# Optimization experiments

Hardware: AMD Instinct MI355X
Metric: run time of the kernel (lower is better)

Reference implementation:

```python
import jax, jax.numpy as jnp
import numpy as np

DIM = 2048
NUM_HEADS = 16
HEAD_DIM = DIM // NUM_HEADS
ROPE_BASE = 10000.0


def _rope_cache(seq_len):
    inv_freq = 1.0 / (ROPE_BASE ** (jnp.arange(0, HEAD_DIM, 2, dtype=jnp.float32) / HEAD_DIM))
    t = jnp.arange(seq_len, dtype=jnp.float32)
    freqs = jnp.einsum('i,j->ij', t, inv_freq)          # [S, HEAD_DIM//2]
    emb = jnp.concatenate([freqs, freqs], axis=-1)       # [S, HEAD_DIM]
    return jnp.cos(emb), jnp.sin(emb)


def _rotate_half(x):
    x1, x2 = jnp.split(x, 2, axis=-1)
    return jnp.concatenate([-x2, x1], axis=-1)


def setup_inputs() -> dict:
    key = jax.random.key(0)
    kx, kq, ko = jax.random.split(key, 3)
    B, S = 2, 2048
    x = jax.random.normal(kx, (B, S, DIM), dtype=jnp.float32)
    # torch nn.Linear(dim, 3*dim) weight has shape [3*dim, dim]; y = x @ W.T
    w_qkv = jax.random.normal(kq, (3 * DIM, DIM), dtype=jnp.float32) * (DIM ** -0.5)
    w_out = jax.random.normal(ko, (DIM, DIM), dtype=jnp.float32) * (DIM ** -0.5)
    return {"x": x, "w_qkv": w_qkv, "w_out": w_out}


def reference(x, w_qkv, w_out):
    B, S, _ = x.shape
    qkv = x @ w_qkv.T                                   # [B, S, 3*DIM]
    q, k, v = jnp.split(qkv, 3, axis=-1)
    def to_heads(t):
        return t.reshape(B, S, NUM_HEADS, HEAD_DIM).transpose(0, 2, 1, 3)  # [B, H, S, d]
    q, k, v = to_heads(q), to_heads(k), to_heads(v)

    cos, sin = _rope_cache(S)                           # [S, d]
    cos = cos[None, None, :, :]
    sin = sin[None, None, :, :]
    q = q * cos + _rotate_half(q) * sin
    k = k * cos + _rotate_half(k) * sin

    scale = HEAD_DIM ** -0.5
    scores = jnp.einsum('bhqd,bhkd->bhqk', q, k) * scale  # [B, H, S, S]
    causal = jnp.tril(jnp.ones((S, S), dtype=bool))
    scores = jnp.where(causal[None, None], scores, -jnp.inf)
    attn = jax.nn.softmax(scores, axis=-1)
    out = jnp.einsum('bhqk,bhkd->bhqd', attn, v)          # [B, H, S, d]
    out = out.transpose(0, 2, 1, 3).reshape(B, S, DIM)
    return out @ w_out.T
```

## Files before the change

### kernel.cpp

```cpp
#include <hip/hip_runtime.h>
#include <cstdint>
#include <cstddef>

#define NHEADS 16
#define HDIM   128
#define BATCH  2
#define SEQ    2048
#define DMODEL 2048
#define MTOT   (BATCH*SEQ)
#define NQKV   (3*DMODEL)

typedef __attribute__((ext_vector_type(8))) __bf16 bf16x8;
typedef __attribute__((ext_vector_type(4))) float f32x4;
typedef __attribute__((ext_vector_type(8))) unsigned short ushort8v;

__device__ __forceinline__ unsigned short f2bf(float f){
  __bf16 h = (__bf16)f;
  return __builtin_bit_cast(unsigned short, h);
}
__device__ __forceinline__ float bf2f(unsigned short s){
  return __uint_as_float(((uint32_t)s) << 16);
}
__device__ __forceinline__ void gload_lds16(const void* src, void* lds_base){
  __builtin_amdgcn_global_load_lds((const __attribute__((address_space(1))) unsigned int*)src,
                                   (__attribute__((address_space(3))) unsigned int*)lds_base,
                                   16, 0, 0);
}

template<int CTRL>
__device__ __forceinline__ float dppmv(float x){
  return __uint_as_float((unsigned)__builtin_amdgcn_update_dpp(
      0, (int)__float_as_uint(x), CTRL, 0xF, 0xF, true));
}
__device__ __forceinline__ float rmax16(float x){
  x = fmaxf(x, dppmv<0x128>(x));
  x = fmaxf(x, dppmv<0x124>(x));
  x = fmaxf(x, dppmv<0x122>(x));
  x = fmaxf(x, dppmv<0x121>(x));
  return x;
}
__device__ __forceinline__ float rsum16(float x){
  x += dppmv<0x128>(x);
  x += dppmv<0x124>(x);
  x += dppmv<0x122>(x);
  x += dppmv<0x121>(x);
  return x;
}

__global__ void cast3_kernel(const float* __restrict__ s0, unsigned short* __restrict__ d0, int n0,
                             const float* __restrict__ s1, unsigned short* __restrict__ d1, int n1,
                             const float* __restrict__ s2, unsigned short* __restrict__ d2, int n2){
  const int stride = gridDim.x*blockDim.x*8;
  const int base = (blockIdx.x*blockDim.x + threadIdx.x)*8;
  #pragma unroll 1
  for (int a = 0; a < 3; ++a){
    const float* s = a==0 ? s0 : (a==1 ? s1 : s2);
    unsigned short* d = a==0 ? d0 : (a==1 ? d1 : d2);
    const int n = a==0 ? n0 : (a==1 ? n1 : n2);
    for (int i = base; i < n; i += stride){
      float4 x = *reinterpret_cast<const float4*>(s + i);
      float4 y = *reinterpret_cast<const float4*>(s + i + 4);
      ushort8v o;
      o[0]=f2bf(x.x); o[1]=f2bf(x.y); o[2]=f2bf(x.z); o[3]=f2bf(x.w);
      o[4]=f2bf(y.x); o[5]=f2bf(y.y); o[6]=f2bf(y.z); o[7]=f2bf(y.w);
      *reinterpret_cast<ushort8v*>(d + i) = o;
    }
  }
}

template<int MODE>
__global__ __launch_bounds__(512, 2) void gemm2(
    const unsigned short* __restrict__ A,
    const unsigned short* __restrict__ Bw,
    float* __restrict__ Cf,
    unsigned short* __restrict__ qo,
    unsigned short* __restrict__ ko,
    unsigned short* __restrict__ vo,
    int M, int N, int K)
{
  __shared__ __align__(16) unsigned short smem[49152];
  auto lds = reinterpret_cast<unsigned short (*)[3][128*64]>(smem);

  const int lane = threadIdx.x & 63;
  const int wid  = threadIdx.x >> 6;
  const int wm = wid >> 2, wn = wid & 3;
  const int hi = lane >> 4;
  const int l15 = lane & 15;

  const int nwg = gridDim.x * gridDim.y;
  const int bid = blockIdx.y * gridDim.x + blockIdx.x;
  const int swz = (bid & 7) * (nwg >> 3) + (bid >> 3);
  const int by = swz & 31;
  const int bx = swz >> 5;
  const int m0 = by * 128;
  const int n0 = bx * 256;

  const int NT = K >> 6;

  auto stage = [&](const unsigned short* base, int row0, int k0, int buf, int slot){
    const int rlo = wid << 4;
    #pragma unroll
    for (int i=0;i<2;++i){
      const int r = rlo + i*8 + (lane>>3);
      const int csrc = ((lane&7) ^ (lane>>3)) << 3;
      gload_lds16(base + (size_t)(row0 + r)*K + k0 + csrc,
                  &lds[buf][slot][(rlo + i*8)*64]);
    }
  };
  auto frag = [&](const unsigned short* h, int r, int s){
    return *reinterpret_cast<const bf16x8*>(h + r*64 + ((s ^ (r&7)) << 3));
  };

  f32x4 acc[4][4];
  #pragma unroll
  for (int i=0;i<4;++i)
    #pragma unroll
    for (int j=0;j<4;++j) acc[i][j] = (f32x4){0.f,0.f,0.f,0.f};

  stage(A,  m0,      0, 0, 0);
  stage(Bw, n0,      0, 0, 1);
  stage(Bw, n0+128,  0, 0, 2);
  if (NT > 1){
    stage(A, m0, 64, 1, 0);
    asm volatile("s_waitcnt vmcnt(2)" ::: "memory");
  } else {
    asm volatile("s_waitcnt vmcnt(0)" ::: "memory");
  }
  __builtin_amdgcn_sched_barrier(0);
  __builtin_amdgcn_s_barrier();

  bf16x8 Ar[4][2];
  bf16x8 Br[2][2];

  auto tile_body = [&](int kt, int cur){
    const int nxt = cur ^ 1;
    const unsigned short* Ah = &lds[cur][0][0];
    const unsigned short* Bh = &lds[cur][1 + (wn>>1)][0];
    const int rbase = (wn & 1) * 64;

    #pragma unroll
    for (int fm=0;fm<4;++fm)
      #pragma unroll
      for (int kk=0;kk<2;++kk)
        Ar[fm][kk] = frag(Ah, wm*64 + fm*16 + l15, kk*4 + hi);
    #pragma unroll
    for (int nf=0;nf<2;++nf)
      #pragma unroll
      for (int kk=0;kk<2;++kk)
        Br[nf][kk] = frag(Bh, rbase + nf*16 + l15, kk*4 + hi);
    if (kt+1 < NT){
      stage(Bw, n0,     (kt+1)*64, nxt, 1);
      stage(Bw, n0+128, (kt+1)*64, nxt, 2);
    }
    asm volatile("s_waitcnt lgkmcnt(8)" ::: "memory");
    __builtin_amdgcn_sched_barrier(0);
    __builtin_amdgcn_s_barrier();
    asm volatile("s_waitcnt lgkmcnt(0)" ::: "memory");
    __builtin_amdgcn_sched_barrier(0);
    __builtin_amdgcn_s_setprio(1);
    #pragma unroll
    for (int fm=0;fm<4;++fm){
      acc[fm][0] = __builtin_amdgcn_mfma_f32_16x16x32_bf16(Ar[fm][0], Br[0][0], acc[fm][0], 0,0,0);
      acc[fm][0] = __builtin_amdgcn_mfma_f32_16x16x32_bf16(Ar[fm][1], Br[0][1], acc[fm][0], 0,0,0);
      acc[fm][1] = __builtin_amdgcn_mfma_f32_16x16x32_bf16(Ar[fm][0], Br[1][0], acc[fm][1], 0,0,0);
      acc[fm][1] = __builtin_amdgcn_mfma_f32_16x16x32_bf16(Ar[fm][1], Br[1][1], acc[fm][1], 0,0,0);
    }
    __builtin_amdgcn_s_setprio(0);
    __builtin_amdgcn_sched_barrier(0);
    __builtin_amdgcn_s_barrier();

    #pragma unroll
    for (int nf=0;nf<2;++nf)
      #pragma unroll
      for (int kk=0;kk<2;++kk)
        Br[nf][kk] = frag(Bh, rbase + 32 + nf*16 + l15, kk*4 + hi);
    if (kt+2 < NT) stage(A, m0, (kt+2)*64, cur, 0);
    __builtin_amdgcn_sched_barrier(0);
    __builtin_amdgcn_s_barrier();
    asm volatile("s_waitcnt lgkmcnt(0)" ::: "memory");
    __builtin_amdgcn_sched_barrier(0);
    __builtin_amdgcn_s_setprio(1);
    #pragma unroll
    for (int fm=0;fm<4;++fm){
      acc[fm][2] = __builtin_amdgcn_mfma_f32_16x16x32_bf16(Ar[fm][0], Br[0][0], acc[fm][2], 0,0,0);
      acc[fm][2] = __builtin_amdgcn_mfma_f32_16x16x32_bf16(Ar[fm][1], Br[0][1], acc[fm][2], 0,0,0);
      acc[fm][3] = __builtin_amdgcn_mfma_f32_16x16x32_bf16(Ar[fm][0], Br[1][0], acc[fm][3], 0,0,0);
      acc[fm][3] = __builtin_amdgcn_mfma_f32_16x16x32_bf16(Ar[fm][1], Br[1][1], acc[fm][3], 0,0,0);
    }
    __builtin_amdgcn_s_setprio(0);
    if (kt+2 < NT)      asm volatile("s_waitcnt vmcnt(2)" ::: "memory");
    else if (kt+1 < NT) asm volatile("s_waitcnt vmcnt(0)" ::: "memory");
    __builtin_amdgcn_sched_barrier(0);
    __builtin_amdgcn_s_barrier();
  };

  for (int kt2 = 0; kt2 < NT; kt2 += 2){
    tile_body(kt2,     0);
    tile_body(kt2 + 1, 1);
  }

  if (MODE == 0 && (n0 >> 11) == 2){
    __builtin_amdgcn_s_barrier();
    unsigned short* trsp = smem;
    #pragma unroll
    for (int fm=0;fm<4;++fm){
      const int srow = wm*64 + fm*16 + hi*4;
      #pragma unroll
      for (int p=0;p<4;++p){
        const int dcol = wn*64 + p*16 + l15;
        f32x4 v = acc[fm][p];
        ushort4 pk;
        pk.x=f2bf(v[0]); pk.y=f2bf(v[1]); pk.z=f2bf(v[2]); pk.w=f2bf(v[3]);
        *reinterpret_cast<ushort4*>(trsp + dcol*136 + srow) = pk;
      }
    }
    __syncthreads();
    const int bb  = m0 >> 11;
    const int ss0 = m0 & 2047;
    const size_t vrow = (size_t)(bb*2048 + (n0 - 4096));
    const int t = threadIdx.x;
    #pragma unroll
    for (int it=0; it<8; ++it){
      const int dl = it*32 + (t>>4);
      const int ch = t & 15;
      ushort8v val = *reinterpret_cast<const ushort8v*>(trsp + dl*136 + ch*8);
      *reinterpret_cast<ushort8v*>(vo + (vrow + dl)*SEQ + ss0 + ch*8) = val;
    }
  } else {
    #pragma unroll
    for (int fm=0;fm<4;++fm){
      const int row0 = m0 + wm*64 + fm*16 + (hi<<2);
      #pragma unroll
      for (int p=0;p<4;++p){
        const int col = n0 + wn*64 + p*16 + l15;
        f32x4 v = acc[fm][p];
        if (MODE == 1){
          #pragma unroll
          for (int r=0;r<4;++r) Cf[(size_t)(row0+r)*N + col] = v[r];
        } else {
          const int part = col >> 11;
          const int hh = (col >> 7) & 15;
          const int d  = col & 127;
          const int bb = row0 >> 11;
          const int ss = row0 & 2047;
          unsigned short* base = (part == 0 ? qo : ko)
                               + ((size_t)(bb*NHEADS+hh)*SEQ + ss)*HDIM + d;
          #pragma unroll
          for (int r=0;r<4;++r) base[r*HDIM] = f2bf(v[r]);
        }
      }
    }
  }
}

__global__ void rope_kernel(unsigned short* __restrict__ qh, unsigned short* __restrict__ kh){
  const int idx = blockIdx.x * blockDim.x + threadIdx.x;
  const int j  = idx & 63;
  const int s  = (idx >> 6) & 2047;
  const int bh = (idx >> 17) & 31;
  const int t  = idx >> 22;
  unsigned short* base = (t ? kh : qh) + ((size_t)bh*SEQ + s)*HDIM;
  const float x1 = bf2f(base[j]);
  const float x2 = bf2f(base[j+64]);
  const float inv = exp2f(-(float)j * (13.287712379549449f/64.f));
  const float ang = (float)s * inv;
  float sn, cs;
  sincosf(ang, &sn, &cs);
  float o1 = x1*cs - x2*sn;
  float o2 = x2*cs + x1*sn;
  const float QSCALE = 0.08838834764831845f * 1.4426950408889634f;
  if (t == 0){ o1 *= QSCALE; o2 *= QSCALE; }
  base[j]    = f2bf(o1);
  base[j+64] = f2bf(o2);
}

__global__ __launch_bounds__(256, 2) void attn_kernel(
    const unsigned short* __restrict__ qh,
    const unsigned short* __restrict__ kh,
    const unsigned short* __restrict__ vT,
    unsigned short* __restrict__ ao)
{
  __shared__ __align__(16) unsigned short Ks[2][64*128];
  __shared__ __align__(16) unsigned short Vs[2][128*64];
  __shared__ __align__(16) unsigned short Ps[4][16*64];

  const int lane = threadIdx.x & 63;
  const int wid  = threadIdx.x >> 6;
  const int hi   = lane >> 4;
  const int l15  = lane & 15;
  const int pr = blockIdx.x;
  const int bh = blockIdx.y;
  const int b_ = bh >> 4, h_ = bh & 15;

  const unsigned short* Qb = qh + (size_t)bh * SEQ * HDIM;
  const unsigned short* Kb = kh + (size_t)bh * SEQ * HDIM;
  const unsigned short* Vb = vT + (size_t)bh * HDIM * SEQ;

  const int qrowf[2] = { pr*64 + wid*16, (31-pr)*64 + wid*16 };

  auto stageKV = [&](int kg, int buf){
    #pragma unroll
    for (int i=0;i<4;++i){
      const int r  = (wid*4+i)*4 + (lane>>4);
      const int cb = ((lane&15)<<4) ^ ((r&7)<<4);
      gload_lds16(Kb + (size_t)(kg*64 + r)*HDIM + (cb>>1), &Ks[buf][0] + (wid*4+i)*512);
    }
    #pragma unroll
    for (int i=0;i<4;++i){
      const int d  = (wid*4+i)*8 + (lane>>3);
      const int cb = ((lane&7)<<4) ^ ((d&7)<<4);
      gload_lds16(Vb + (size_t)d*SEQ + kg*64 + (cb>>1), &Vs[buf][0] + (wid*4+i)*512);
    }
  };

  bf16x8 qf[2][4];
  #pragma unroll
  for (int fi=0; fi<2; ++fi){
    const int qr = qrowf[fi] + l15;
    #pragma unroll
    for (int ks = 0; ks < 4; ++ks)
      qf[fi][ks] = *reinterpret_cast<const bf16x8*>(Qb + (size_t)qr*HDIM + ks*32 + hi*8);
  }

  f32x4 oacc[2][8];
  #pragma unroll
  for (int fi=0;fi<2;++fi)
    #pragma unroll
    for (int t=0;t<8;++t) oacc[fi][t] = (f32x4){0.f,0.f,0.f,0.f};
  float mrun[2][4], lrun[2][4];
  #pragma unroll
  for (int fi=0;fi<2;++fi)
    #pragma unroll
    for (int r=0;r<4;++r){ mrun[fi][r] = -3.0e38f; lrun[fi][r] = 0.f; }

  const int nkt = 32 - pr;

  stageKV(0, 0);
  __syncthreads();

  for (int kt = 0; kt < nkt; ++kt){
    const int cur = kt & 1;
    if (kt + 1 < nkt) stageKV(kt + 1, cur ^ 1);

    const bool lo_act = (kt <= pr);

    f32x4 sacc[2][4];
    #pragma unroll
    for (int fi=0;fi<2;++fi)
      #pragma unroll
      for (int nt=0;nt<4;++nt) sacc[fi][nt] = (f32x4){0.f,0.f,0.f,0.f};
    __builtin_amdgcn_s_setprio(1);
    #pragma unroll
    for (int nt=0;nt<4;++nt){
      const int krow = nt*16 + l15;
      bf16x8 kf[4];
      #pragma unroll
      for (int ks=0;ks<4;++ks){
        const int cb = (ks*64 + (hi<<4)) ^ ((krow&7)<<4);
        kf[ks] = *reinterpret_cast<const bf16x8*>(&Ks[cur][0] + krow*128 + (cb>>1));
      }
      #pragma unroll
      for (int ks=0;ks<4;++ks)
        sacc[1][nt] = __builtin_amdgcn_mfma_f32_16x16x32_bf16(qf[1][ks], kf[ks], sacc[1][nt], 0,0,0);
      if (lo_act){
        #pragma unroll
        for (int ks=0;ks<4;++ks)
          sacc[0][nt] = __builtin_amdgcn_mfma_f32_16x16x32_bf16(qf[0][ks], kf[ks], sacc[0][nt], 0,0,0);
      }
    }
    __builtin_amdgcn_s_setprio(0);

    char* pb = (char*)&Ps[wid][0];
    #pragma unroll
    for (int fi=0; fi<2; ++fi){
      if (fi == 0 && !lo_act) continue;

      if (kt*64 + 63 > qrowf[fi]){
        #pragma unroll
        for (int nt=0;nt<4;++nt){
          const int key = kt*64 + nt*16 + l15;
          #pragma unroll
          for (int r=0;r<4;++r){
            const int qr = qrowf[fi] + hi*4 + r;
            if (key > qr) sacc[fi][nt][r] = -1.0e30f;
          }
        }
      }

      float fac[4];
      #pragma unroll
      for (int r=0;r<4;++r){
        float mx = fmaxf(fmaxf(sacc[fi][0][r], sacc[fi][1][r]),
                         fmaxf(sacc[fi][2][r], sacc[fi][3][r]));
        mx = rmax16(mx);
        const float mnew = fmaxf(mrun[fi][r], mx);
        fac[r] = exp2f(mrun[fi][r] - mnew);
        mrun[fi][r] = mnew;
        float ps = 0.f;
        #pragma unroll
        for (int nt=0;nt<4;++nt){
          const float p = exp2f(sacc[fi][nt][r] - mnew);
          sacc[fi][nt][r] = p;
          ps += p;
        }
        ps = rsum16(ps);
        lrun[fi][r] = lrun[fi][r]*fac[r] + ps;
      }
      #pragma unroll
      for (int t=0;t<8;++t)
        #pragma unroll
        for (int r=0;r<4;++r) oacc[fi][t][r] *= fac[r];

      #pragma unroll
      for (int nt=0;nt<4;++nt){
        const int keyb = (nt*16 + l15) << 1;
        #pragma unroll
        for (int r=0;r<4;++r){
          const int prow = hi*4 + r;
          *(unsigned short*)(pb + prow*128 + (keyb ^ ((prow&7)<<4))) = f2bf(sacc[fi][nt][r]);
        }
      }
      asm volatile("s_waitcnt lgkmcnt(0)" ::: "memory");
      __builtin_amdgcn_sched_barrier(0);

      bf16x8 pa[2];
      {
        const int prow = l15;
        #pragma unroll
        for (int ks=0;ks<2;++ks){
          const int pcb = (ks*64 + (hi<<4)) ^ ((prow&7)<<4);
          pa[ks] = *reinterpret_cast<const bf16x8*>(pb + prow*128 + pcb);
        }
      }
      __builtin_amdgcn_s_setprio(1);
      #pragma unroll
      for (int ks=0;ks<2;++ks){
        #pragma unroll
        for (int t=0;t<8;++t){
          const int drow = t*16 + l15;
          const int vcb = (ks*64 + (hi<<4)) ^ ((drow&7)<<4);
          bf16x8 vb = *reinterpret_cast<const bf16x8*>(&Vs[cur][0] + drow*64 + (vcb>>1));
          oacc[fi][t] = __builtin_amdgcn_mfma_f32_16x16x32_bf16(pa[ks], vb, oacc[fi][t], 0,0,0);
        }
      }
      __builtin_amdgcn_s_setprio(0);
    }

    __syncthreads();
  }

  #pragma unroll
  for (int fi=0;fi<2;++fi){
    float linv[4];
    #pragma unroll
    for (int r=0;r<4;++r) linv[r] = 1.0f / lrun[fi][r];
    #pragma unroll
    for (int t=0;t<8;++t){
      const int col = h_*HDIM + t*16 + l15;
      #pragma unroll
      for (int r=0;r<4;++r){
        const int s_ = qrowf[fi] + hi*4 + r;
        ao[(size_t)(b_*SEQ + s_)*DMODEL + col] = f2bf(oacc[fi][t][r] * linv[r]);
      }
    }
  }
}

extern "C" void kernel_launch(void* const* d_in, const int* in_sizes, int n_in,
                              void* d_out, int out_size, void* d_ws, size_t ws_size,
                              hipStream_t stream)
{
  const float* x     = (const float*)d_in[0];
  const float* w_qkv = (const float*)d_in[1];
  const float* w_out = (const float*)d_in[2];
  float* out = (float*)d_out;

  unsigned short* xb    = (unsigned short*)d_ws;
  unsigned short* wqkvb = xb    + (size_t)MTOT*DMODEL;
  unsigned short* woutb = wqkvb + (size_t)NQKV*DMODEL;
  unsigned short* qhb   = woutb + (size_t)DMODEL*DMODEL;
  unsigned short* khb   = qhb   + (size_t)MTOT*DMODEL;
  unsigned short* vtb   = khb   + (size_t)MTOT*DMODEL;
  unsigned short* aob   = vtb   + (size_t)MTOT*DMODEL;

  hipLaunchKernelGGL(cast3_kernel, dim3(1024), dim3(256), 0, stream,
                     x, xb, MTOT*DMODEL, w_qkv, wqkvb, NQKV*DMODEL, w_out, woutb, DMODEL*DMODEL);
  hipLaunchKernelGGL((gemm2<0>), dim3(NQKV/256, MTOT/128), dim3(512), 0, stream,
                     xb, wqkvb, (float*)nullptr, qhb, khb, vtb, MTOT, NQKV, DMODEL);
  hipLaunchKernelGGL(rope_kernel, dim3((2*BATCH*NHEADS*SEQ*64)/256), dim3(256), 0, stream, qhb, khb);
  hipLaunchKernelGGL(attn_kernel, dim3(16, BATCH*NHEADS), dim3(256), 0, stream, qhb, khb, vtb, aob);
  hipLaunchKernelGGL((gemm2<1>), dim3(DMODEL/256, MTOT/128), dim3(512), 0, stream,
                     aob, woutb, out, (unsigned short*)nullptr, (unsigned short*)nullptr,
                     (unsigned short*)nullptr, MTOT, DMODEL, DMODEL);
}
```

Measured before the change: 262.6 us.

## Add pipelined 128x128 output-projection GEMM and lazy softmax rescaling

Adds a dedicated output-projection GEMM kernel with 128x128 tiles, 256 threads, double-buffered LDS staging via direct global-to-LDS loads, split MFMA phases with priority hints and an XCD-aware block swizzle. It replaces the previous 256-wide gemm2<1> launch so the 4096x2048 output GEMM uses more workgroups. Separately, the attention softmax now skips the running-max rescale of the O accumulator and row sum unless some row's max grows by more than 8 (log2 units), which removes per-tile multiplies at the cost of letting unnormalized exponentials grow up to 2^8. The swizzle hardcodes 32 row-blocks, so the new GEMM assumes M=4096.

```diff
diff --git a/kernel.cpp b/kernel.cpp
--- a/kernel.cpp
+++ b/kernel.cpp
@@ -249,6 +249,140 @@
           for (int r=0;r<4;++r) base[r*HDIM] = f2bf(v[r]);
         }
       }
+    }
+  }
+}
+
+__global__ __launch_bounds__(256, 2) void gemm_op(
+    const unsigned short* __restrict__ A,
+    const unsigned short* __restrict__ Bw,
+    float* __restrict__ Cf,
+    int M, int N, int K)
+{
+  __shared__ __align__(16) unsigned short smem[2][2][128*64];
+  const int lane = threadIdx.x & 63;
+  const int wid  = threadIdx.x >> 6;
+  const int wm = wid >> 1, wn = wid & 1;
+  const int hi = lane >> 4;
+  const int l15 = lane & 15;
+
+  const int nwg = gridDim.x * gridDim.y;
+  const int bid = blockIdx.y * gridDim.x + blockIdx.x;
+  const int swz = (bid & 7) * (nwg >> 3) + (bid >> 3);
+  const int by = swz & 31;
+  const int bx = swz >> 5;
+  const int m0 = by * 128;
+  const int n0 = bx * 128;
+
+  const int NT = K >> 6;
+
+  auto stage = [&](const unsigned short* base, int row0, int k0, int buf, int slot){
+    const int rlo = wid << 5;
+    #pragma unroll
+    for (int i=0;i<4;++i){
+      const int r = rlo + i*8 + (lane>>3);
+      const int csrc = ((lane&7) ^ (lane>>3)) << 3;
+      gload_lds16(base + (size_t)(row0 + r)*K + k0 + csrc,
+                  &smem[buf][slot][(rlo + i*8)*64]);
+    }
+  };
+  auto frag = [&](const unsigned short* h, int r, int s){
+    return *reinterpret_cast<const bf16x8*>(h + r*64 + ((s ^ (r&7)) << 3));
+  };
+
+  f32x4 acc[4][4];
+  #pragma unroll
+  for (int i=0;i<4;++i)
+    #pragma unroll
+    for (int j=0;j<4;++j) acc[i][j] = (f32x4){0.f,0.f,0.f,0.f};
+
+  stage(A,  m0, 0, 0, 0);
+  stage(Bw, n0, 0, 0, 1);
+  if (NT > 1){
+    stage(A, m0, 64, 1, 0);
+    asm volatile("s_waitcnt vmcnt(4)" ::: "memory");
+  } else {
+    asm volatile("s_waitcnt vmcnt(0)" ::: "memory");
+  }
+  __builtin_amdgcn_sched_barrier(0);
+  __builtin_amdgcn_s_barrier();
+
+  bf16x8 Ar[4][2];
+  bf16x8 Br[2][2];
+
+  auto tile_body = [&](int kt, int cur){
+    const int nxt = cur ^ 1;
+    const unsigned short* Ah = &smem[cur][0][0];
+    const unsigned short* Bh = &smem[cur][1][0];
+    const int rbase = wn * 64;
+
+    #pragma unroll
+    for (int fm=0;fm<4;++fm)
+      #pragma unroll
+      for (int kk=0;kk<2;++kk)
+        Ar[fm][kk] = frag(Ah, wm*64 + fm*16 + l15, kk*4 + hi);
+    #pragma unroll
+    for (int nf=0;nf<2;++nf)
+      #pragma unroll
+      for (int kk=0;kk<2;++kk)
+        Br[nf][kk] = frag(Bh, rbase + nf*16 + l15, kk*4 + hi);
+    if (kt+1 < NT) stage(Bw, n0, (kt+1)*64, nxt, 1);
+    asm volatile("s_waitcnt lgkmcnt(8)" ::: "memory");
+    __builtin_amdgcn_sched_barrier(0);
+    __builtin_amdgcn_s_barrier();
+    asm volatile("s_waitcnt lgkmcnt(0)" ::: "memory");
+    __builtin_amdgcn_sched_barrier(0);
+    __builtin_amdgcn_s_setprio(1);
+    #pragma unroll
+    for (int fm=0;fm<4;++fm){
+      acc[fm][0] = __builtin_amdgcn_mfma_f32_16x16x32_bf16(Ar[fm][0], Br[0][0], acc[fm][0], 0,0,0);
+      acc[fm][0] = __builtin_amdgcn_mfma_f32_16x16x32_bf16(Ar[fm][1], Br[0][1], acc[fm][0], 0,0,0);
+      acc[fm][1] = __builtin_amdgcn_mfma_f32_16x16x32_bf16(Ar[fm][0], Br[1][0], acc[fm][1], 0,0,0);
+      acc[fm][1] = __builtin_amdgcn_mfma_f32_16x16x32_bf16(Ar[fm][1], Br[1][1], acc[fm][1], 0,0,0);
+    }
+    __builtin_amdgcn_s_setprio(0);
+    __builtin_amdgcn_sched_barrier(0);
+    __builtin_amdgcn_s_barrier();
+
+    #pragma unroll
+    for (int nf=0;nf<2;++nf)
+      #pragma unroll
+      for (int kk=0;kk<2;++kk)
+        Br[nf][kk] = frag(Bh, rbase + 32 + nf*16 + l15, kk*4 + hi);
+    if (kt+2 < NT) stage(A, m0, (kt+2)*64, cur, 0);
+    __builtin_amdgcn_sched_barrier(0);
+    __builtin_amdgcn_s_barrier();
+    asm volatile("s_waitcnt lgkmcnt(0)" ::: "memory");
+    __builtin_amdgcn_sched_barrier(0);
+    __builtin_amdgcn_s_setprio(1);
+    #pragma unroll
+    for (int fm=0;fm<4;++fm){
+      acc[fm][2] = __builtin_amdgcn_mfma_f32_16x16x32_bf16(Ar[fm][0], Br[0][0], acc[fm][2], 0,0,0);
+      acc[fm][2] = __builtin_amdgcn_mfma_f32_16x16x32_bf16(Ar[fm][1], Br[0][1], acc[fm][2], 0,0,0);
+      acc[fm][3] = __builtin_amdgcn_mfma_f32_16x16x32_bf16(Ar[fm][0], Br[1][0], acc[fm][3], 0,0,0);
+      acc[fm][3] = __builtin_amdgcn_mfma_f32_16x16x32_bf16(Ar[fm][1], Br[1][1], acc[fm][3], 0,0,0);
+    }
+    __builtin_amdgcn_s_setprio(0);
+    if (kt+2 < NT)      asm volatile("s_waitcnt vmcnt(4)" ::: "memory");
+    else if (kt+1 < NT) asm volatile("s_waitcnt vmcnt(0)" ::: "memory");
+    __builtin_amdgcn_sched_barrier(0);
+    __builtin_amdgcn_s_barrier();
+  };
+
+  for (int kt2 = 0; kt2 < NT; kt2 += 2){
+    tile_body(kt2,     0);
+    tile_body(kt2 + 1, 1);
+  }
+
+  #pragma unroll
+  for (int fm=0;fm<4;++fm){
+    const int row0 = m0 + wm*64 + fm*16 + (hi<<2);
+    #pragma unroll
+    for (int p=0;p<4;++p){
+      const int col = n0 + wn*64 + p*16 + l15;
+      f32x4 v = acc[fm][p];
+      #pragma unroll
+      for (int r=0;r<4;++r) Cf[(size_t)(row0+r)*N + col] = v[r];
     }
   }
 }
@@ -387,29 +521,41 @@
         }
       }
 
-      float fac[4];
+      float mx[4]; float need = 0.f;
       #pragma unroll
       for (int r=0;r<4;++r){
-        float mx = fmaxf(fmaxf(sacc[fi][0][r], sacc[fi][1][r]),
+        float m_ = fmaxf(fmaxf(sacc[fi][0][r], sacc[fi][1][r]),
                          fmaxf(sacc[fi][2][r], sacc[fi][3][r]));
-        mx = rmax16(mx);
-        const float mnew = fmaxf(mrun[fi][r], mx);
-        fac[r] = exp2f(mrun[fi][r] - mnew);
-        mrun[fi][r] = mnew;
+        m_ = rmax16(m_);
+        mx[r] = m_;
+        need = fmaxf(need, m_ - mrun[fi][r]);
+      }
+      if (!__all(need <= 8.0f)){
+        float fac[4];
+        #pragma unroll
+        for (int r=0;r<4;++r){
+          const float mnew = fmaxf(mrun[fi][r], mx[r]);
+          fac[r] = exp2f(mrun[fi][r] - mnew);
+          mrun[fi][r] = mnew;
+          lrun[fi][r] *= fac[r];
+        }
+        #pragma unroll
+        for (int t=0;t<8;++t)
+          #pragma unroll
+          for (int r=0;r<4;++r) oacc[fi][t][r] *= fac[r];
+      }
+      #pragma unroll
+      for (int r=0;r<4;++r){
         float ps = 0.f;
         #pragma unroll
         for (int nt=0;nt<4;++nt){
-          const float p = exp2f(sacc[fi][nt][r] - mnew);
+          const float p = exp2f(sacc[fi][nt][r] - mrun[fi][r]);
           sacc[fi][nt][r] = p;
           ps += p;
         }
         ps = rsum16(ps);
-        lrun[fi][r] = lrun[fi][r]*fac[r] + ps;
-      }
-      #pragma unroll
-      for (int t=0;t<8;++t)
-        #pragma unroll
-        for (int r=0;r<4;++r) oacc[fi][t][r] *= fac[r];
+        lrun[fi][r] += ps;
+      }
 
       #pragma unroll
       for (int nt=0;nt<4;++nt){
@@ -489,7 +635,6 @@
                      xb, wqkvb, (float*)nullptr, qhb, khb, vtb, MTOT, NQKV, DMODEL);
   hipLaunchKernelGGL(rope_kernel, dim3((2*BATCH*NHEADS*SEQ*64)/256), dim3(256), 0, stream, qhb, khb);
   hipLaunchKernelGGL(attn_kernel, dim3(16, BATCH*NHEADS), dim3(256), 0, stream, qhb, khb, vtb, aob);
-  hipLaunchKernelGGL((gemm2<1>), dim3(DMODEL/256, MTOT/128), dim3(512), 0, stream,
-                     aob, woutb, out, (unsigned short*)nullptr, (unsigned short*)nullptr,
-                     (unsigned short*)nullptr, MTOT, DMODEL, DMODEL);
-}
+  hipLaunchKernelGGL(gemm_op, dim3(DMODEL/128, MTOT/128), dim3(256), 0, stream,
+                     aob, woutb, out, MTOT, DMODEL, DMODEL);
+}
```

Result: no change. 262.3 us (-0.1%).
